# Kernel tuning notes

Hardware: AMD Instinct MI355X
Metric: run time of the kernel (lower is better)

Reference implementation:

```python
import jax, jax.numpy as jnp
import numpy as np


def apply_rotary_emb(x, freqs_cis):
    # x: [B, N, H, Dh], freqs_cis: [N, Dh//2, 2]
    B, N, H, Dh = x.shape
    x2 = x.reshape(B, N, H, Dh // 2, 2)
    f = freqs_cis[None, :, None]  # [1, N, 1, Dh//2, 2]
    real = x2[..., 0] * f[..., 0] - x2[..., 1] * f[..., 1]
    imag = x2[..., 1] * f[..., 0] + x2[..., 0] * f[..., 1]
    out = jnp.stack([real, imag], axis=-1)
    return out.reshape(B, N, H, Dh).astype(x.dtype)


def setup_inputs() -> dict:
    key = jax.random.key(0)
    k1, k2, k3, k4 = jax.random.split(key, 4)
    B, N, dim, n_head = 2, 2048, 2048, 16
    head_dim = dim // n_head
    x = jax.random.normal(k1, (B, N, dim), dtype=jnp.float32)
    # realistic rotary freqs (cos/sin), though random also works for correctness
    pos = jnp.arange(N, dtype=jnp.float32)[:, None]
    inv_freq = 1.0 / (10000.0 ** (jnp.arange(0, head_dim, 2, dtype=jnp.float32) / head_dim))
    ang = pos * inv_freq[None, :]  # [N, Dh//2]
    freqs_cis = jnp.stack([jnp.cos(ang), jnp.sin(ang)], axis=-1)  # [N, Dh//2, 2]
    wqkv = jax.random.normal(k2, (dim, 3 * dim), dtype=jnp.float32) * (dim ** -0.5)
    wo = jax.random.normal(k3, (dim, dim), dtype=jnp.float32) * (dim ** -0.5)
    return {"x": x, "freqs_cis": freqs_cis, "wqkv": wqkv, "wo": wo}


def reference(x, freqs_cis, wqkv, wo):
    B, N, dim = x.shape
    n_head = 16
    head_dim = dim // n_head
    qkv = x @ wqkv  # [B, N, 3*dim]
    q, k, v = jnp.split(qkv, 3, axis=-1)
    q = q.reshape(B, N, n_head, head_dim)
    k = k.reshape(B, N, n_head, head_dim)
    v = v.reshape(B, N, n_head, head_dim)
    q = apply_rotary_emb(q, freqs_cis)
    k = apply_rotary_emb(k, freqs_cis)
    scale = 1.0 / jnp.sqrt(jnp.asarray(head_dim, dtype=q.dtype))
    scores = jnp.einsum('bqhd,bkhd->bhqk', q, k) * scale
    attn = jax.nn.softmax(scores, axis=-1)
    out = jnp.einsum('bhqk,bkhd->bqhd', attn, v).reshape(B, N, dim)
    return out @ wo
```

## Files before the change

### kernel.cpp

```cpp
#include <hip/hip_runtime.h>
#include <hip/hip_bf16.h>
#include <stdint.h>

typedef __attribute__((ext_vector_type(8))) short bf16x8;
typedef __attribute__((ext_vector_type(4))) float f32x4;
typedef __attribute__((ext_vector_type(4))) unsigned short u16x4;
typedef __attribute__((ext_vector_type(8))) unsigned short u16x8;

#define DEV __device__ __forceinline__

DEV unsigned short f2bf(float f) {
  union { __hip_bfloat16 h; unsigned short u; } cv;
  cv.h = __float2bfloat16(f);
  return cv.u;
}

DEV void gload_lds16(const void* g, void* l) {
  __builtin_amdgcn_global_load_lds(
      (__attribute__((address_space(1))) void*)(uintptr_t)g,
      (__attribute__((address_space(3))) void*)(uint32_t)(uintptr_t)l,
      16, 0, 0);
}

__global__ __launch_bounds__(256) void k_convert(const float* __restrict__ in,
                                                 unsigned short* __restrict__ out,
                                                 int n8) {
  int i = blockIdx.x * 256 + threadIdx.x;
  if (i >= n8) return;
  const float4* p = (const float4*)in + (size_t)i * 2;
  float4 a = p[0], b = p[1];
  u16x8 o;
  o[0] = f2bf(a.x); o[1] = f2bf(a.y); o[2] = f2bf(a.z); o[3] = f2bf(a.w);
  o[4] = f2bf(b.x); o[5] = f2bf(b.y); o[6] = f2bf(b.z); o[7] = f2bf(b.w);
  *((u16x8*)out + (size_t)i) = o;
}

__global__ __launch_bounds__(256) void k_transpose_bf16(const float* __restrict__ in,
                                                        unsigned short* __restrict__ out,
                                                        int R, int C) {
  __shared__ float tile[32][33];
  const int t = threadIdx.x;
  const int c0 = blockIdx.x * 32, r0 = blockIdx.y * 32;
  {
    int r = t >> 3, c4 = (t & 7) * 4;
    float4 v = *(const float4*)&in[(size_t)(r0 + r) * C + c0 + c4];
    tile[r][c4] = v.x; tile[r][c4 + 1] = v.y; tile[r][c4 + 2] = v.z; tile[r][c4 + 3] = v.w;
  }
  __syncthreads();
  int c = t >> 3, r4 = (t & 7) * 4;
  u16x4 o;
  o[0] = f2bf(tile[r4 + 0][c]); o[1] = f2bf(tile[r4 + 1][c]);
  o[2] = f2bf(tile[r4 + 2][c]); o[3] = f2bf(tile[r4 + 3][c]);
  *(u16x4*)&out[(size_t)(c0 + c) * R + r0 + r4] = o;
}

__global__ __launch_bounds__(512, 2) void k_gemm_qkv(
    const unsigned short* __restrict__ A,
    const unsigned short* __restrict__ Bt,
    unsigned short* __restrict__ qb,
    unsigned short* __restrict__ kb,
    unsigned short* __restrict__ vt,
    const float* __restrict__ freqs) {
  constexpr int Kdim = 2048;
  __shared__ unsigned short As[2][256 * 64];
  __shared__ unsigned short Bs[2][256 * 64];
  const int t = threadIdx.x;
  const int lane = t & 63, wid = t >> 6;
  const int l15 = lane & 15, l4 = (lane >> 4) & 3;
  const int wm = wid >> 2, wn = wid & 3;
  const int bid = blockIdx.x;
  const int wg = (bid & 7) * 48 + (bid >> 3);
  const int by = wg & 15, bx = wg >> 4;
  const int m0 = by * 256, n0 = bx * 256;

  f32x4 acc[8][4];
#pragma unroll
  for (int i = 0; i < 8; i++)
#pragma unroll
    for (int j = 0; j < 4; j++) acc[i][j] = (f32x4)0.f;

  auto stageHalf = [&](unsigned short* tile, const unsigned short* src, int half) {
#pragma unroll
    for (int cb = 0; cb < 2; cb++) {
      int slotu = half * 1024 + cb * 512 + wid * 64;
      int slot = slotu + lane;
      int row = slot >> 3, cc = slot & 7;
      int cg = cc ^ (row & 7);
      gload_lds16(src + (size_t)row * Kdim + cg * 8, tile + slotu * 8);
    }
  };

  auto rdA = [&](int buf, int mh, bf16x8 (&f)[4][2]) {
#pragma unroll
    for (int mi = 0; mi < 4; mi++) {
      int row = wm * 128 + mh * 64 + mi * 16 + l15;
#pragma unroll
      for (int kk = 0; kk < 2; kk++) {
        int c = (kk * 4 + l4) ^ (row & 7);
        f[mi][kk] = *(const bf16x8*)&As[buf][row * 64 + c * 8];
      }
    }
  };
  auto rdB = [&](int buf, int nh, bf16x8 (&f)[2][2]) {
#pragma unroll
    for (int ni = 0; ni < 2; ni++) {
      int row = wn * 64 + nh * 32 + ni * 16 + l15;
#pragma unroll
      for (int kk = 0; kk < 2; kk++) {
        int c = (kk * 4 + l4) ^ (row & 7);
        f[ni][kk] = *(const bf16x8*)&Bs[buf][row * 64 + c * 8];
      }
    }
  };
  auto mmaQ = [&](bf16x8 (&af)[4][2], bf16x8 (&bf)[2][2], int mib, int nib) {
    __builtin_amdgcn_s_setprio(1);
#pragma unroll
    for (int kk = 0; kk < 2; kk++)
#pragma unroll
      for (int mi = 0; mi < 4; mi++)
#pragma unroll
        for (int ni = 0; ni < 2; ni++)
          acc[mib + mi][nib + ni] = __builtin_amdgcn_mfma_f32_16x16x32_bf16(
              af[mi][kk], bf[ni][kk], acc[mib + mi][nib + ni], 0, 0, 0);
    __builtin_amdgcn_s_setprio(0);
  };

  const unsigned short* Abase = A + (size_t)m0 * Kdim;
  const unsigned short* Bbase = Bt + (size_t)n0 * Kdim;

  stageHalf(As[0], Abase, 0);
  stageHalf(As[0], Abase, 1);
  stageHalf(Bs[0], Bbase, 0);
  stageHalf(Bs[0], Bbase, 1);
  __syncthreads();

  bf16x8 af[4][2], b0[2][2], b1[2][2];
  for (int j = 0; j < 32; j++) {
    const int buf = j & 1;
    const unsigned short* An = Abase + (j + 1) * 64;
    const unsigned short* Bn = Bbase + (j + 1) * 64;
    const bool st = (j < 31);
    rdA(buf, 0, af);
    rdB(buf, 0, b0);
    if (st) stageHalf(As[buf ^ 1], An, 0);
    __builtin_amdgcn_s_barrier();
    asm volatile("s_waitcnt lgkmcnt(0)" ::: "memory");
    mmaQ(af, b0, 0, 0);
    __builtin_amdgcn_s_barrier();
    rdB(buf, 1, b1);
    if (st) stageHalf(As[buf ^ 1], An, 1);
    __builtin_amdgcn_s_barrier();
    asm volatile("s_waitcnt lgkmcnt(0)" ::: "memory");
    mmaQ(af, b1, 0, 2);
    __builtin_amdgcn_s_barrier();
    rdA(buf, 1, af);
    if (st) stageHalf(Bs[buf ^ 1], Bn, 0);
    __builtin_amdgcn_s_barrier();
    asm volatile("s_waitcnt lgkmcnt(0)" ::: "memory");
    mmaQ(af, b0, 4, 0);
    __builtin_amdgcn_s_barrier();
    if (st) stageHalf(Bs[buf ^ 1], Bn, 1);
    __builtin_amdgcn_s_barrier();
    mmaQ(af, b1, 4, 2);
    __syncthreads();
  }

#pragma unroll
  for (int mi = 0; mi < 8; mi++) {
    int rowb = m0 + wm * 128 + mi * 16 + l4 * 4;
    int b = rowb >> 11;
    int tok0 = rowb & 2047;
#pragma unroll
    for (int ni = 0; ni < 4; ni++) {
      int col = n0 + wn * 64 + ni * 16 + l15;
      int sec = col >> 11;
      int h = (col >> 7) & 15;
      int dh = col & 127;
      if (sec == 2) {
        u16x4 o;
#pragma unroll
        for (int r = 0; r < 4; r++) o[r] = f2bf(acc[mi][ni][r]);
        *(u16x4*)&vt[((size_t)(b * 16 + h) * 128 + dh) * 2048 + tok0] = o;
      } else {
        unsigned short* dst = (sec == 0) ? qb : kb;
        int dh2 = dh >> 1;
        int odd = dh & 1;
#pragma unroll
        for (int r = 0; r < 4; r++) {
          float v = acc[mi][ni][r];
          float p = __shfl_xor(v, 1, 64);
          float2 cs = *(const float2*)&freqs[((size_t)(tok0 + r) * 64 + dh2) * 2];
          float o = odd ? (v * cs.x + p * cs.y) : (v * cs.x - p * cs.y);
          dst[((size_t)(b * 16 + h) * 2048 + tok0 + r) * 128 + dh] = f2bf(o);
        }
      }
    }
  }
}

__global__ __launch_bounds__(256) void k_gemm_out(
    const unsigned short* __restrict__ A,
    const unsigned short* __restrict__ Bt,
    int Kdim, int Nn,
    float* __restrict__ Cout) {
  __shared__ unsigned short As[128 * 64];
  __shared__ unsigned short Bs[128 * 64];
  const int t = threadIdx.x;
  const int lane = t & 63, wid = t >> 6;
  const int l15 = lane & 15, l4 = lane >> 4;
  const int m0 = blockIdx.y * 128, n0 = blockIdx.x * 128;
  const int wr = (wid >> 1) * 64, wc = (wid & 1) * 64;

  f32x4 acc[4][4];
#pragma unroll
  for (int i = 0; i < 4; i++)
#pragma unroll
    for (int j = 0; j < 4; j++) acc[i][j] = (f32x4)0.f;

  for (int k0 = 0; k0 < Kdim; k0 += 64) {
    __syncthreads();
#pragma unroll
    for (int j = 0; j < 4; j++) {
      int slotbase = j * 256 + wid * 64;
      int slot = slotbase + lane;
      int row = slot >> 3, cc = slot & 7;
      int cg = cc ^ (row & 7);
      gload_lds16(A + (size_t)(m0 + row) * Kdim + k0 + cg * 8, &As[slotbase * 8]);
      gload_lds16(Bt + (size_t)(n0 + row) * Kdim + k0 + cg * 8, &Bs[slotbase * 8]);
    }
    __syncthreads();
#pragma unroll
    for (int kk = 0; kk < 2; kk++) {
      bf16x8 af[4], bfr[4];
#pragma unroll
      for (int mi = 0; mi < 4; mi++) {
        int row = wr + mi * 16 + l15;
        int c = (kk * 4 + l4) ^ (row & 7);
        af[mi] = *(const bf16x8*)&As[row * 64 + c * 8];
      }
#pragma unroll
      for (int ni = 0; ni < 4; ni++) {
        int row = wc + ni * 16 + l15;
        int c = (kk * 4 + l4) ^ (row & 7);
        bfr[ni] = *(const bf16x8*)&Bs[row * 64 + c * 8];
      }
#pragma unroll
      for (int mi = 0; mi < 4; mi++)
#pragma unroll
        for (int ni = 0; ni < 4; ni++)
          acc[mi][ni] = __builtin_amdgcn_mfma_f32_16x16x32_bf16(af[mi], bfr[ni],
                                                                acc[mi][ni], 0, 0, 0);
    }
  }

#pragma unroll
  for (int mi = 0; mi < 4; mi++) {
    int rowb = m0 + wr + mi * 16 + l4 * 4;
#pragma unroll
    for (int ni = 0; ni < 4; ni++) {
      int col = n0 + wc + ni * 16 + l15;
#pragma unroll
      for (int r = 0; r < 4; r++)
        Cout[(size_t)(rowb + r) * Nn + col] = acc[mi][ni][r];
    }
  }
}

__global__ __launch_bounds__(256, 2) void k_attn(
    const unsigned short* __restrict__ qb,
    const unsigned short* __restrict__ kb,
    const unsigned short* __restrict__ vt,
    unsigned short* __restrict__ ao) {
  __shared__ unsigned short Ks[2][64 * 128];
  __shared__ unsigned short Vs[2][64 * 128];
  __shared__ unsigned short Ps[4][32 * 64];
  const int t = threadIdx.x;
  const int lane = t & 63, wid = t >> 6;
  const int l15 = lane & 15, l4 = lane >> 4;
  const int qt0 = blockIdx.x * 128;
  const int bh = blockIdx.y;
  const unsigned short* qbase = qb + (size_t)bh * 2048 * 128;
  const unsigned short* kbase = kb + (size_t)bh * 2048 * 128;
  const unsigned short* vbase = vt + (size_t)bh * 128 * 2048;

  bf16x8 qf[2][4];
#pragma unroll
  for (int mi = 0; mi < 2; mi++) {
    int qrow = qt0 + wid * 32 + mi * 16 + l15;
#pragma unroll
    for (int dk = 0; dk < 4; dk++)
      qf[mi][dk] = *(const bf16x8*)&qbase[(size_t)qrow * 128 + dk * 32 + l4 * 8];
  }

  f32x4 O[2][8];
#pragma unroll
  for (int mi = 0; mi < 2; mi++)
#pragma unroll
    for (int df = 0; df < 8; df++) O[mi][df] = (f32x4)0.f;
  float lsum[2][4];
#pragma unroll
  for (int mi = 0; mi < 2; mi++)
#pragma unroll
    for (int r = 0; r < 4; r++) lsum[mi][r] = 0.f;

  const float scale = 0.08838834764831845f;

  auto STAGE = [&](int kv0, int buf) {
#pragma unroll
    for (int j = 0; j < 4; j++) {
      int slotbase = j * 256 + wid * 64;
      int slot = slotbase + lane;
      int rowk = slot >> 4, ck = slot & 15;
      gload_lds16(&kbase[(size_t)(kv0 + rowk) * 128 + (ck ^ (rowk & 7)) * 8],
                  &Ks[buf][slotbase * 8]);
      int rowv = slot >> 3, cv = slot & 7;
      gload_lds16(&vbase[(size_t)rowv * 2048 + kv0 + (cv ^ (rowv & 7)) * 8],
                  &Vs[buf][slotbase * 8]);
    }
  };

  STAGE(0, 0);
  __syncthreads();

  for (int ti = 0; ti < 32; ti++) {
    const int cur = ti & 1;
    if (ti < 31) STAGE((ti + 1) * 64, cur ^ 1);

    f32x4 s[2][4];
#pragma unroll
    for (int mi = 0; mi < 2; mi++)
#pragma unroll
      for (int ni = 0; ni < 4; ni++) s[mi][ni] = (f32x4)0.f;
#pragma unroll
    for (int dk = 0; dk < 4; dk++) {
      bf16x8 kf[4];
#pragma unroll
      for (int ni = 0; ni < 4; ni++) {
        int row = ni * 16 + l15;
        int c = (dk * 4 + l4) ^ (row & 7);
        kf[ni] = *(const bf16x8*)&Ks[cur][row * 128 + c * 8];
      }
#pragma unroll
      for (int mi = 0; mi < 2; mi++)
#pragma unroll
        for (int ni = 0; ni < 4; ni++)
          s[mi][ni] = __builtin_amdgcn_mfma_f32_16x16x32_bf16(qf[mi][dk], kf[ni],
                                                              s[mi][ni], 0, 0, 0);
    }

    unsigned short* pbase = &Ps[wid][0];
#pragma unroll
    for (int mi = 0; mi < 2; mi++)
#pragma unroll
      for (int ni = 0; ni < 4; ni++) {
        int col = ni * 16 + l15;
#pragma unroll
        for (int r = 0; r < 4; r++) {
          float p = __expf(s[mi][ni][r] * scale);
          lsum[mi][r] += p;
          int rowp = mi * 16 + l4 * 4 + r;
          pbase[rowp * 64 + (((col >> 3) ^ (rowp & 7)) << 3) + (col & 7)] = f2bf(p);
        }
      }

    bf16x8 pf[2][2];
#pragma unroll
    for (int mi = 0; mi < 2; mi++)
#pragma unroll
      for (int kk = 0; kk < 2; kk++) {
        int row = mi * 16 + l15;
        int c = (kk * 4 + l4) ^ (row & 7);
        pf[mi][kk] = *(const bf16x8*)&pbase[row * 64 + c * 8];
      }

#pragma unroll
    for (int df = 0; df < 8; df++) {
      bf16x8 vf[2];
#pragma unroll
      for (int kk = 0; kk < 2; kk++) {
        int row = df * 16 + l15;
        int c = (kk * 4 + l4) ^ (row & 7);
        vf[kk] = *(const bf16x8*)&Vs[cur][row * 64 + c * 8];
      }
#pragma unroll
      for (int mi = 0; mi < 2; mi++)
#pragma unroll
        for (int kk = 0; kk < 2; kk++)
          O[mi][df] = __builtin_amdgcn_mfma_f32_16x16x32_bf16(pf[mi][kk], vf[kk],
                                                              O[mi][df], 0, 0, 0);
    }

    __syncthreads();
  }

  float inv[2][4];
#pragma unroll
  for (int mi = 0; mi < 2; mi++)
#pragma unroll
    for (int r = 0; r < 4; r++) {
      float v = lsum[mi][r];
      v += __shfl_xor(v, 1, 64);
      v += __shfl_xor(v, 2, 64);
      v += __shfl_xor(v, 4, 64);
      v += __shfl_xor(v, 8, 64);
      inv[mi][r] = 1.0f / v;
    }

  const int b = bh >> 4, h = bh & 15;
#pragma unroll
  for (int mi = 0; mi < 2; mi++)
#pragma unroll
    for (int df = 0; df < 8; df++)
#pragma unroll
      for (int r = 0; r < 4; r++) {
        int tok = qt0 + wid * 32 + mi * 16 + l4 * 4 + r;
        ao[((size_t)(b * 2048 + tok)) * 2048 + h * 128 + df * 16 + l15] =
            f2bf(O[mi][df][r] * inv[mi][r]);
      }
}

extern "C" void kernel_launch(void* const* d_in, const int* in_sizes, int n_in,
                              void* d_out, int out_size, void* d_ws, size_t ws_size,
                              hipStream_t stream) {
  const float* x     = (const float*)d_in[0];
  const float* freqs = (const float*)d_in[1];
  const float* wqkv  = (const float*)d_in[2];
  const float* wo    = (const float*)d_in[3];
  float* out = (float*)d_out;

  char* ws = (char*)d_ws;
  unsigned short* xb    = (unsigned short*)(ws + 0);
  unsigned short* wqkvT = (unsigned short*)(ws + 16777216);
  unsigned short* woT   = (unsigned short*)(ws + 41943040);
  unsigned short* qb    = (unsigned short*)(ws + 50331648);
  unsigned short* kb    = (unsigned short*)(ws + 67108864);
  unsigned short* vt    = (unsigned short*)(ws + 83886080);
  unsigned short* ao    = (unsigned short*)(ws + 100663296);

  k_convert<<<dim3(4096), dim3(256), 0, stream>>>(x, xb, 1048576);
  k_transpose_bf16<<<dim3(192, 64), dim3(256), 0, stream>>>(wqkv, wqkvT, 2048, 6144);
  k_transpose_bf16<<<dim3(64, 64), dim3(256), 0, stream>>>(wo, woT, 2048, 2048);

  k_gemm_qkv<<<dim3(384), dim3(512), 0, stream>>>(xb, wqkvT, qb, kb, vt, freqs);

  k_attn<<<dim3(16, 32), dim3(256), 0, stream>>>(qb, kb, vt, ao);

  k_gemm_out<<<dim3(16, 32), dim3(256), 0, stream>>>(ao, woT, 2048, 2048, out);
}
```

Measured before the change: 283.3 us.

## Split QKV GEMM K-tile into K-half LDS units with finer vmcnt pipelining

Reorganizes the QKV projection GEMM's LDS layout so each 64-wide K tile is stored as two separate 32-wide K-half units, staged independently. The main loop now iterates over K-halves, loading full 4x4 fragment sets per phase. It replaces the trailing __syncthreads with explicit vmcnt(4) waits so global->LDS loads of the next halves can stay in flight across phases. The XOR swizzle is removed (rows are now 64 bytes), which may introduce LDS bank conflicts on the fragment reads.

```diff
diff --git a/kernel.cpp b/kernel.cpp
--- a/kernel.cpp
+++ b/kernel.cpp
@@ -62,8 +62,8 @@
     unsigned short* __restrict__ vt,
     const float* __restrict__ freqs) {
   constexpr int Kdim = 2048;
-  __shared__ unsigned short As[2][256 * 64];
-  __shared__ unsigned short Bs[2][256 * 64];
+  __shared__ unsigned short As[2][16384];
+  __shared__ unsigned short Bs[2][16384];
   const int t = threadIdx.x;
   const int lane = t & 63, wid = t >> 6;
   const int l15 = lane & 15, l4 = (lane >> 4) & 3;
@@ -79,90 +79,98 @@
 #pragma unroll
     for (int j = 0; j < 4; j++) acc[i][j] = (f32x4)0.f;
 
-  auto stageHalf = [&](unsigned short* tile, const unsigned short* src, int half) {
+  auto stageU = [&](unsigned short* dstUnit, const unsigned short* src, int khalf) {
 #pragma unroll
     for (int cb = 0; cb < 2; cb++) {
-      int slotu = half * 1024 + cb * 512 + wid * 64;
+      int slotu = cb * 512 + wid * 64;
       int slot = slotu + lane;
-      int row = slot >> 3, cc = slot & 7;
-      int cg = cc ^ (row & 7);
-      gload_lds16(src + (size_t)row * Kdim + cg * 8, tile + slotu * 8);
+      int row = slot >> 2, ch = slot & 3;
+      gload_lds16(src + (size_t)row * Kdim + khalf * 32 + ch * 8,
+                  dstUnit + slotu * 8);
     }
   };
 
-  auto rdA = [&](int buf, int mh, bf16x8 (&f)[4][2]) {
+  auto rdA2 = [&](int buf, int kk, int mh, bf16x8 (&f)[4]) {
+    const unsigned short* base = &As[buf][kk * 8192];
 #pragma unroll
     for (int mi = 0; mi < 4; mi++) {
       int row = wm * 128 + mh * 64 + mi * 16 + l15;
-#pragma unroll
-      for (int kk = 0; kk < 2; kk++) {
-        int c = (kk * 4 + l4) ^ (row & 7);
-        f[mi][kk] = *(const bf16x8*)&As[buf][row * 64 + c * 8];
-      }
+      f[mi] = *(const bf16x8*)&base[row * 32 + l4 * 8];
     }
   };
-  auto rdB = [&](int buf, int nh, bf16x8 (&f)[2][2]) {
-#pragma unroll
-    for (int ni = 0; ni < 2; ni++) {
-      int row = wn * 64 + nh * 32 + ni * 16 + l15;
-#pragma unroll
-      for (int kk = 0; kk < 2; kk++) {
-        int c = (kk * 4 + l4) ^ (row & 7);
-        f[ni][kk] = *(const bf16x8*)&Bs[buf][row * 64 + c * 8];
-      }
+  auto rdB2 = [&](int buf, int kk, bf16x8 (&f)[4]) {
+    const unsigned short* base = &Bs[buf][kk * 8192];
+#pragma unroll
+    for (int ni = 0; ni < 4; ni++) {
+      int row = wn * 64 + ni * 16 + l15;
+      f[ni] = *(const bf16x8*)&base[row * 32 + l4 * 8];
     }
   };
-  auto mmaQ = [&](bf16x8 (&af)[4][2], bf16x8 (&bf)[2][2], int mib, int nib) {
+  auto mmaP = [&](bf16x8 (&a4)[4], bf16x8 (&b4)[4], int mib) {
     __builtin_amdgcn_s_setprio(1);
 #pragma unroll
-    for (int kk = 0; kk < 2; kk++)
-#pragma unroll
-      for (int mi = 0; mi < 4; mi++)
-#pragma unroll
-        for (int ni = 0; ni < 2; ni++)
-          acc[mib + mi][nib + ni] = __builtin_amdgcn_mfma_f32_16x16x32_bf16(
-              af[mi][kk], bf[ni][kk], acc[mib + mi][nib + ni], 0, 0, 0);
+    for (int mi = 0; mi < 4; mi++)
+#pragma unroll
+      for (int ni = 0; ni < 4; ni++)
+        acc[mib + mi][ni] = __builtin_amdgcn_mfma_f32_16x16x32_bf16(
+            a4[mi], b4[ni], acc[mib + mi][ni], 0, 0, 0);
     __builtin_amdgcn_s_setprio(0);
   };
 
   const unsigned short* Abase = A + (size_t)m0 * Kdim;
   const unsigned short* Bbase = Bt + (size_t)n0 * Kdim;
 
-  stageHalf(As[0], Abase, 0);
-  stageHalf(As[0], Abase, 1);
-  stageHalf(Bs[0], Bbase, 0);
-  stageHalf(Bs[0], Bbase, 1);
-  __syncthreads();
-
-  bf16x8 af[4][2], b0[2][2], b1[2][2];
+  stageU(&As[0][0], Abase, 0);
+  stageU(&Bs[0][0], Bbase, 0);
+  stageU(&As[0][8192], Abase, 1);
+  stageU(&Bs[0][8192], Bbase, 1);
+  asm volatile("s_waitcnt vmcnt(4)" ::: "memory");
+  __builtin_amdgcn_s_barrier();
+
+  bf16x8 a4[4], b4[4];
   for (int j = 0; j < 32; j++) {
     const int buf = j & 1;
     const unsigned short* An = Abase + (j + 1) * 64;
     const unsigned short* Bn = Bbase + (j + 1) * 64;
+    unsigned short* Ad = &As[buf ^ 1][0];
+    unsigned short* Bd = &Bs[buf ^ 1][0];
     const bool st = (j < 31);
-    rdA(buf, 0, af);
-    rdB(buf, 0, b0);
-    if (st) stageHalf(As[buf ^ 1], An, 0);
+
+    rdA2(buf, 0, 0, a4);
+    rdB2(buf, 0, b4);
+    if (st) stageU(Ad, An, 0);
     __builtin_amdgcn_s_barrier();
     asm volatile("s_waitcnt lgkmcnt(0)" ::: "memory");
-    mmaQ(af, b0, 0, 0);
-    __builtin_amdgcn_s_barrier();
-    rdB(buf, 1, b1);
-    if (st) stageHalf(As[buf ^ 1], An, 1);
+    __builtin_amdgcn_sched_barrier(0);
+    mmaP(a4, b4, 0);
+    __builtin_amdgcn_s_barrier();
+
+    rdA2(buf, 0, 1, a4);
+    if (st) stageU(Bd, Bn, 0);
     __builtin_amdgcn_s_barrier();
     asm volatile("s_waitcnt lgkmcnt(0)" ::: "memory");
-    mmaQ(af, b1, 0, 2);
-    __builtin_amdgcn_s_barrier();
-    rdA(buf, 1, af);
-    if (st) stageHalf(Bs[buf ^ 1], Bn, 0);
+    __builtin_amdgcn_sched_barrier(0);
+    mmaP(a4, b4, 4);
+    asm volatile("s_waitcnt vmcnt(4)" ::: "memory");
+    __builtin_amdgcn_s_barrier();
+
+    rdA2(buf, 1, 0, a4);
+    rdB2(buf, 1, b4);
+    if (st) stageU(Ad + 8192, An, 1);
     __builtin_amdgcn_s_barrier();
     asm volatile("s_waitcnt lgkmcnt(0)" ::: "memory");
-    mmaQ(af, b0, 4, 0);
-    __builtin_amdgcn_s_barrier();
-    if (st) stageHalf(Bs[buf ^ 1], Bn, 1);
-    __builtin_amdgcn_s_barrier();
-    mmaQ(af, b1, 4, 2);
-    __syncthreads();
+    __builtin_amdgcn_sched_barrier(0);
+    mmaP(a4, b4, 0);
+    __builtin_amdgcn_s_barrier();
+
+    rdA2(buf, 1, 1, a4);
+    if (st) stageU(Bd + 8192, Bn, 1);
+    __builtin_amdgcn_s_barrier();
+    asm volatile("s_waitcnt lgkmcnt(0)" ::: "memory");
+    __builtin_amdgcn_sched_barrier(0);
+    mmaP(a4, b4, 4);
+    asm volatile("s_waitcnt vmcnt(4)" ::: "memory");
+    __builtin_amdgcn_s_barrier();
   }
 
 #pragma unroll
```

Result: no change. 287.9 us (+1.6%).
